# Kernel tuning notes

Measured on AMD Instinct MI355X. Metric: run time of the kernel, lower is better.

Reference implementation:

```python
import jax, jax.numpy as jnp
import numpy as np

NEG_SLOPE = 0.2
EPS = 1e-16


def setup_inputs() -> dict:
    key = jax.random.key(0)
    k1, k2, k3, k4, k5 = jax.random.split(key, 5)
    N, E, F_IN, H, C = 100000, 1600000, 128, 4, 32
    x = jax.random.normal(k1, (N, F_IN), dtype=jnp.float32)
    edge_index = jax.random.randint(k2, (2, E), 0, N, dtype=jnp.int64)
    W = jax.random.normal(k3, (F_IN, H * C), dtype=jnp.float32) * (1.0 / np.sqrt(F_IN))
    att_src = jax.random.normal(k4, (H, C), dtype=jnp.float32) * 0.1
    att_dst = jax.random.normal(k5, (H, C), dtype=jnp.float32) * 0.1
    bias = jnp.zeros((H * C,), dtype=jnp.float32)
    return {"x": x, "edge_index": edge_index, "W": W, "att_src": att_src,
            "att_dst": att_dst, "bias": bias}


def reference(x, edge_index, W, att_src, att_dst, bias):
    N = x.shape[0]
    H, C = att_src.shape
    # PyG GATConv default: add self-loops
    loops = jnp.arange(N, dtype=edge_index.dtype)
    src = jnp.concatenate([edge_index[0], loops])  # [E+N]
    dst = jnp.concatenate([edge_index[1], loops])  # [E+N]

    h = (x @ W).reshape(N, H, C)                  # [N,H,C]
    a_src = jnp.einsum('nhc,hc->nh', h, att_src)  # [N,H]
    a_dst = jnp.einsum('nhc,hc->nh', h, att_dst)  # [N,H]

    e = a_src[src] + a_dst[dst]                   # [E',H]
    e = jax.nn.leaky_relu(e, NEG_SLOPE)

    # segment softmax over destination nodes (numerically stable)
    m = jax.ops.segment_max(e, dst, num_segments=N)      # [N,H]
    p = jnp.exp(e - m[dst])                               # [E',H]
    s = jax.ops.segment_sum(p, dst, num_segments=N)       # [N,H]
    alpha = p / (s[dst] + EPS)                             # [E',H]

    msg = h[src] * alpha[:, :, None]                       # [E',H,C]
    out = jax.ops.segment_sum(msg, dst, num_segments=N)   # [N,H,C]
    return out.reshape(N, H * C) + bias
```

## Files before the change

kernel.cpp:

```cpp
#include <hip/hip_runtime.h>
#include <stdint.h>


#define SLOT 64
#define CNTS 16

typedef __attribute__((ext_vector_type(8))) _Float16 h8;
typedef __attribute__((ext_vector_type(4))) float    f4x;

__device__ __forceinline__ float b2f(unsigned short u) {
    union { unsigned int i; float f; } v; v.i = ((unsigned int)u) << 16; return v.f;
}
__device__ __forceinline__ unsigned short f2b(float f) {
    union { float f; unsigned int i; } v; v.f = f;
    unsigned int i = v.i;
    unsigned int r = (i + 0x7FFFu + ((i >> 16) & 1u)) >> 16;
    return (unsigned short)r;
}
__device__ __forceinline__ unsigned short f2h(float f) {
    union { _Float16 h; unsigned short u; } v; v.h = (_Float16)f; return v.u;
}
__device__ __forceinline__ float h2f(unsigned short u) {
    union { _Float16 h; unsigned short u; } v; v.u = u; return (float)v.h;
}

__global__ void k_detect(const int* __restrict__ eidx, const unsigned int* __restrict__ xw,
                         int* flags) {
    __shared__ int nz, bf;
    if (threadIdx.x == 0) { nz = 0; bf = 0; }
    __syncthreads();
    int bad = 0;
    for (int i = threadIdx.x; i < 1024; i += 256)
        if (eidx[2 * i + 1] != 0) bad = 1;
    if (bad) atomicOr(&nz, 1);
    int hits = 0;
    for (int i = threadIdx.x; i < 4096; i += 256) {
        unsigned int e = (xw[i] >> 7) & 0xFFu;
        if (e >= 0x60u && e < 0xA0u) ++hits;
    }
    atomicAdd(&bf, hits);
    __syncthreads();
    if (threadIdx.x == 0) {
        flags[0] = (nz == 0) ? 1 : 0;
        flags[1] = (bf > 3072) ? 1 : 0;
    }
}

__device__ __forceinline__ int edge_at(const int* idx32, const long long* idx64,
                                       int is64, long long pos) {
    return is64 ? (int)idx64[pos] : idx32[pos];
}

__global__ void k_prep(const void* __restrict__ Wv, const void* __restrict__ asv,
                       const void* __restrict__ adv, const void* __restrict__ bv,
                       const int* __restrict__ flags,
                       _Float16* __restrict__ Wth, _Float16* __restrict__ Wtl,
                       float* __restrict__ attf , float* __restrict__ biasf ) {
    int isbf = flags[1];
    int tid = blockIdx.x * 256 + threadIdx.x;
    for (int i = tid; i < 16384; i += gridDim.x * 256) {
        int col = i >> 7, k = i & 127;
        float w = isbf ? b2f(((const unsigned short*)Wv)[k * 128 + col])
                       : ((const float*)Wv)[k * 128 + col];
        unsigned short hi = f2h(w);
        unsigned short lo = f2h(w - h2f(hi));
        ((unsigned short*)Wth)[i] = hi;
        ((unsigned short*)Wtl)[i] = lo;
    }
    if (blockIdx.x == 0) {
        for (int i = threadIdx.x; i < 128; i += 256) {
            attf[i]       = isbf ? b2f(((const unsigned short*)asv)[i]) : ((const float*)asv)[i];
            attf[128 + i] = isbf ? b2f(((const unsigned short*)adv)[i]) : ((const float*)adv)[i];
            biasf[i]      = isbf ? b2f(((const unsigned short*)bv)[i]) : ((const float*)bv)[i];
        }
    }
}

__global__ __launch_bounds__(256) void k_gemm_scatter(
    const void* __restrict__ xv,
    const _Float16* __restrict__ Wth, const _Float16* __restrict__ Wtl,
    const float* __restrict__ attf, const int* __restrict__ flags,
    unsigned short* __restrict__ hbf, float* __restrict__ asf,
    float* __restrict__ adf, int N,
    const int* __restrict__ idx32, const long long* __restrict__ idx64,
    int* __restrict__ cnt, int* __restrict__ esrc, int E, int Gg, int Gs) {
    __shared__ unsigned short xsh[64 * 128];
    __shared__ unsigned short xsl[64 * 128];
    int role = blockIdx.x & 1, rb = blockIdx.x >> 1;
    int tid = threadIdx.x;

    if (role == 1) {
        if (rb >= Gs) return;
        int is64 = flags[0];
        int base = (rb * 256 + tid) * 4;
        if (base + 3 < E) {
            int s0, s1, s2, s3, d0, d1, d2, d3;
            if (is64) {
                s0 = (int)idx64[base];     s1 = (int)idx64[base + 1];
                s2 = (int)idx64[base + 2]; s3 = (int)idx64[base + 3];
                d0 = (int)idx64[(long long)E + base];     d1 = (int)idx64[(long long)E + base + 1];
                d2 = (int)idx64[(long long)E + base + 2]; d3 = (int)idx64[(long long)E + base + 3];
            } else if ((E & 3) == 0) {
                int4 sv = *(const int4*)(idx32 + base);
                int4 dv = *(const int4*)(idx32 + E + base);
                s0 = sv.x; s1 = sv.y; s2 = sv.z; s3 = sv.w;
                d0 = dv.x; d1 = dv.y; d2 = dv.z; d3 = dv.w;
            } else {
                s0 = idx32[base];     s1 = idx32[base + 1];
                s2 = idx32[base + 2]; s3 = idx32[base + 3];
                d0 = idx32[E + base];     d1 = idx32[E + base + 1];
                d2 = idx32[E + base + 2]; d3 = idx32[E + base + 3];
            }
            int p0 = atomicAdd(&cnt[(size_t)d0 * CNTS], 1);
            int p1 = atomicAdd(&cnt[(size_t)d1 * CNTS], 1);
            int p2 = atomicAdd(&cnt[(size_t)d2 * CNTS], 1);
            int p3 = atomicAdd(&cnt[(size_t)d3 * CNTS], 1);
            if (p0 < SLOT) esrc[(size_t)d0 * SLOT + p0] = s0;
            if (p1 < SLOT) esrc[(size_t)d1 * SLOT + p1] = s1;
            if (p2 < SLOT) esrc[(size_t)d2 * SLOT + p2] = s2;
            if (p3 < SLOT) esrc[(size_t)d3 * SLOT + p3] = s3;
        } else {
            for (int e = base; e < E; ++e) {
                int s = edge_at(idx32, idx64, is64, e);
                int d = edge_at(idx32, idx64, is64, (long long)E + e);
                int p = atomicAdd(&cnt[(size_t)d * CNTS], 1);
                if (p < SLOT) esrc[(size_t)d * SLOT + p] = s;
            }
        }
        return;
    }

    if (rb >= Gg) return;
    int r0 = rb * 64;
    int isbf = flags[1];
    int w = tid >> 6;
    int lane = tid & 63;
    int li = lane & 15;
    int g  = lane >> 4;
    int c0 = w * 32;

    h8 Bh[2][4], Bl[2][4];
#pragma unroll
    for (int t = 0; t < 2; ++t)
#pragma unroll
        for (int s = 0; s < 4; ++s) {
            size_t o = (size_t)(c0 + 16 * t + li) * 128 + 32 * s + 8 * g;
            Bh[t][s] = *(const h8*)(Wth + o);
            Bl[t][s] = *(const h8*)(Wtl + o);
        }

#pragma unroll
    for (int it = 0; it < 4; ++it) {
        int idx = it * 2048 + tid * 8;
        int r = idx >> 7, k = idx & 127;
        int gr = r0 + r; if (gr >= N) gr = N - 1;
        float v[8];
        if (isbf) {
            uint4 raw = *(const uint4*)((const unsigned short*)xv + (size_t)gr * 128 + k);
            v[0] = b2f((unsigned short)(raw.x & 0xFFFFu)); v[1] = b2f((unsigned short)(raw.x >> 16));
            v[2] = b2f((unsigned short)(raw.y & 0xFFFFu)); v[3] = b2f((unsigned short)(raw.y >> 16));
            v[4] = b2f((unsigned short)(raw.z & 0xFFFFu)); v[5] = b2f((unsigned short)(raw.z >> 16));
            v[6] = b2f((unsigned short)(raw.w & 0xFFFFu)); v[7] = b2f((unsigned short)(raw.w >> 16));
        } else {
            const float* xf = (const float*)xv;
            float4 a = *(const float4*)(xf + (size_t)gr * 128 + k);
            float4 b = *(const float4*)(xf + (size_t)gr * 128 + k + 4);
            v[0] = a.x; v[1] = a.y; v[2] = a.z; v[3] = a.w;
            v[4] = b.x; v[5] = b.y; v[6] = b.z; v[7] = b.w;
        }
        uint4 PH, PL;
        unsigned int ph[4], pl[4];
#pragma unroll
        for (int jj = 0; jj < 4; ++jj) {
            unsigned short h0 = f2h(v[2 * jj]), h1 = f2h(v[2 * jj + 1]);
            unsigned short l0 = f2h(v[2 * jj] - h2f(h0));
            unsigned short l1 = f2h(v[2 * jj + 1] - h2f(h1));
            ph[jj] = (unsigned int)h0 | ((unsigned int)h1 << 16);
            pl[jj] = (unsigned int)l0 | ((unsigned int)l1 << 16);
        }
        PH.x = ph[0]; PH.y = ph[1]; PH.z = ph[2]; PH.w = ph[3];
        PL.x = pl[0]; PL.y = pl[1]; PL.z = pl[2]; PL.w = pl[3];
        int off = r * 256 + ((2 * k) ^ ((r & 7) << 4));
        *(uint4*)((char*)xsh + off) = PH;
        *(uint4*)((char*)xsl + off) = PL;
    }
    __syncthreads();

    f4x acc[4][2];
#pragma unroll
    for (int m = 0; m < 4; ++m)
#pragma unroll
        for (int t = 0; t < 2; ++t) acc[m][t] = (f4x){0.f, 0.f, 0.f, 0.f};

#pragma unroll
    for (int s = 0; s < 4; ++s) {
#pragma unroll
        for (int m = 0; m < 4; ++m) {
            int row = 16 * m + li;
            int kb = (32 * s + 8 * g) * 2;
            int off = row * 256 + (kb ^ ((row & 7) << 4));
            h8 ah = *(const h8*)((const char*)xsh + off);
            h8 al = *(const h8*)((const char*)xsl + off);
#pragma unroll
            for (int t = 0; t < 2; ++t) {
                acc[m][t] = __builtin_amdgcn_mfma_f32_16x16x32_f16(ah, Bh[t][s], acc[m][t], 0, 0, 0);
                acc[m][t] = __builtin_amdgcn_mfma_f32_16x16x32_f16(al, Bh[t][s], acc[m][t], 0, 0, 0);
                acc[m][t] = __builtin_amdgcn_mfma_f32_16x16x32_f16(ah, Bl[t][s], acc[m][t], 0, 0, 0);
            }
        }
    }

    float at_s0 = attf[c0 + li],       at_s1 = attf[c0 + 16 + li];
    float at_d0 = attf[128 + c0 + li], at_d1 = attf[128 + c0 + 16 + li];
#pragma unroll
    for (int m = 0; m < 4; ++m) {
        float s1v[4], s2v[4];
#pragma unroll
        for (int j = 0; j < 4; ++j) {
            s1v[j] = acc[m][0][j] * at_s0 + acc[m][1][j] * at_s1;
            s2v[j] = acc[m][0][j] * at_d0 + acc[m][1][j] * at_d1;
        }
#pragma unroll
        for (int j = 0; j < 4; ++j) {
#pragma unroll
            for (int msk = 1; msk < 16; msk <<= 1) {
                s1v[j] += __shfl_xor(s1v[j], msk);
                s2v[j] += __shfl_xor(s2v[j], msk);
            }
        }
        if (li == 0) {
#pragma unroll
            for (int j = 0; j < 4; ++j) {
                int gr = r0 + 16 * m + 4 * g + j;
                if (gr < N) {
                    asf[(size_t)gr * 4 + w] = s1v[j];
                    adf[(size_t)gr * 4 + w] = s2v[j];
                }
            }
        }
    }

    __syncthreads();
#pragma unroll
    for (int m = 0; m < 4; ++m)
#pragma unroll
        for (int t = 0; t < 2; ++t)
#pragma unroll
            for (int j = 0; j < 4; ++j)
                xsh[(16 * m + 4 * g + j) * 128 + c0 + 16 * t + li] = f2b(acc[m][t][j]);
    __syncthreads();
#pragma unroll
    for (int it = 0; it < 4; ++it) {
        int u = it * 2048 + tid * 8;
        int r = u >> 7, k = u & 127;
        int gr = r0 + r;
        if (gr < N)
            *(uint4*)(hbf + (size_t)gr * 128 + k) = *(const uint4*)(xsh + u);
    }
}

__global__ __launch_bounds__(256) void k_aggregate(
    const unsigned short* __restrict__ hbf,
    const float* __restrict__ asf, const float* __restrict__ adf,
    const int* __restrict__ cnt, const int* __restrict__ esrc,
    const int* __restrict__ idx32, const long long* __restrict__ idx64,
    const float* __restrict__ biasf, const int* __restrict__ flags,
    void* __restrict__ outv, int N, int E) {
    __shared__ float p_sh_all[4][SLOT * 4];
    __shared__ int   s_sh_all[4][SLOT];
    int wid = threadIdx.x >> 6;
    int lane = threadIdx.x & 63;
    int n = blockIdx.x * 4 + wid;
    if (n >= N) n = N - 1;
    float* p_sh = p_sh_all[wid];
    int*   s_sh = s_sh_all[wid];
    int head = lane >> 4;

    int deg = cnt[(size_t)n * CNTS];
    float4 adv = *(const float4*)(adf + (size_t)n * 4);
    bool fb = (deg > SLOT - 1);

    float p0 = 0.f, p1 = 0.f, p2 = 0.f, p3 = 0.f;
    if (!fb && lane <= deg) {
        int s = (lane == 0) ? n : esrc[(size_t)n * SLOT + lane - 1];
        float4 av = *(const float4*)(asf + (size_t)s * 4);
        float e0 = av.x + adv.x; e0 = fmaxf(e0, 0.2f * e0); p0 = __expf(e0);
        float e1 = av.y + adv.y; e1 = fmaxf(e1, 0.2f * e1); p1 = __expf(e1);
        float e2 = av.z + adv.z; e2 = fmaxf(e2, 0.2f * e2); p2 = __expf(e2);
        float e3 = av.w + adv.w; e3 = fmaxf(e3, 0.2f * e3); p3 = __expf(e3);
        s_sh[lane] = s;
        p_sh[lane * 4 + 0] = p0; p_sh[lane * 4 + 1] = p1;
        p_sh[lane * 4 + 2] = p2; p_sh[lane * 4 + 3] = p3;
    }
    __syncthreads();

    float b0 = biasf[2 * lane], b1 = biasf[2 * lane + 1];
    float a0 = 0.f, a1 = 0.f, invh;

    if (!fb) {
        float ps0 = p0, ps1 = p1, ps2 = p2, ps3 = p3;
#pragma unroll
        for (int m = 1; m < 64; m <<= 1) {
            ps0 += __shfl_xor(ps0, m);
            ps1 += __shfl_xor(ps1, m);
            ps2 += __shfl_xor(ps2, m);
            ps3 += __shfl_xor(ps3, m);
        }
        float den = head == 0 ? ps0 : head == 1 ? ps1 : head == 2 ? ps2 : ps3;
        invh = 1.0f / (den + 1e-16f);

        int tot = deg + 1;
        int i = 0;
        for (; i + 3 < tot; i += 4) {
            int s0 = s_sh[i], s1 = s_sh[i + 1], s2 = s_sh[i + 2], s3 = s_sh[i + 3];
            float q0 = p_sh[i * 4 + head],       q1 = p_sh[(i + 1) * 4 + head];
            float q2 = p_sh[(i + 2) * 4 + head], q3 = p_sh[(i + 3) * 4 + head];
            unsigned int v0 = *(const unsigned int*)(hbf + (size_t)s0 * 128 + 2 * lane);
            unsigned int v1 = *(const unsigned int*)(hbf + (size_t)s1 * 128 + 2 * lane);
            unsigned int v2 = *(const unsigned int*)(hbf + (size_t)s2 * 128 + 2 * lane);
            unsigned int v3 = *(const unsigned int*)(hbf + (size_t)s3 * 128 + 2 * lane);
            a0 += q0 * b2f((unsigned short)v0) + q1 * b2f((unsigned short)v1)
                + q2 * b2f((unsigned short)v2) + q3 * b2f((unsigned short)v3);
            a1 += q0 * b2f((unsigned short)(v0 >> 16)) + q1 * b2f((unsigned short)(v1 >> 16))
                + q2 * b2f((unsigned short)(v2 >> 16)) + q3 * b2f((unsigned short)(v3 >> 16));
        }
        for (; i < tot; ++i) {
            int s0 = s_sh[i];
            float q0 = p_sh[i * 4 + head];
            unsigned int v0 = *(const unsigned int*)(hbf + (size_t)s0 * 128 + 2 * lane);
            a0 += q0 * b2f((unsigned short)v0);
            a1 += q0 * b2f((unsigned short)(v0 >> 16));
        }
    } else {
        int is64 = flags[0];
        float adh = head == 0 ? adv.x : head == 1 ? adv.y : head == 2 ? adv.z : adv.w;
        float den = 0.f;
        {
            float ev = asf[(size_t)n * 4 + head] + adh; ev = fmaxf(ev, 0.2f * ev);
            float p = __expf(ev);
            unsigned int v = *(const unsigned int*)(hbf + (size_t)n * 128 + 2 * lane);
            den += p;
            a0 += p * b2f((unsigned short)v);
            a1 += p * b2f((unsigned short)(v >> 16));
        }
        for (int e = 0; e < E; ++e) {
            int d = edge_at(idx32, idx64, is64, (long long)E + e);
            if (d == n) {
                int s = edge_at(idx32, idx64, is64, e);
                float ev = asf[(size_t)s * 4 + head] + adh; ev = fmaxf(ev, 0.2f * ev);
                float p = __expf(ev);
                unsigned int v = *(const unsigned int*)(hbf + (size_t)s * 128 + 2 * lane);
                den += p;
                a0 += p * b2f((unsigned short)v);
                a1 += p * b2f((unsigned short)(v >> 16));
            }
        }
        invh = 1.0f / (den + 1e-16f);
    }

    a0 = a0 * invh + b0;
    a1 = a1 * invh + b1;
    if (flags[1]) {
        unsigned int pk = (unsigned int)f2b(a0) | ((unsigned int)f2b(a1) << 16);
        ((unsigned int*)outv)[(size_t)n * 64 + lane] = pk;
    } else {
        float2 f2; f2.x = a0; f2.y = a1;
        *(float2*)((float*)outv + (size_t)n * 128 + 2 * lane) = f2;
    }
}

extern "C" void kernel_launch(void* const* d_in, const int* in_sizes, int n_in,
                              void* d_out, int out_size, void* d_ws, size_t ws_size,
                              hipStream_t stream) {
    const void*      xv    = d_in[0];
    const int*       idx32 = (const int*)d_in[1];
    const long long* idx64 = (const long long*)d_in[1];

    int N = in_sizes[0] / 128;
    int E = in_sizes[1] / 2;

    char* ws = (char*)d_ws;
    size_t o = 0;
    auto alloc = [&](size_t bytes) {
        size_t r = o; o += (bytes + 255) & ~(size_t)255; return r;
    };
    unsigned short* hbf = (unsigned short*)(ws + alloc((size_t)N * 128 * 2));
    _Float16* Wth = (_Float16*)(ws + alloc(16384 * 2));
    _Float16* Wtl = (_Float16*)(ws + alloc(16384 * 2));
    float* attf  = (float*)(ws + alloc(256 * 4));
    float* biasf = (float*)(ws + alloc(128 * 4));
    float* asf   = (float*)(ws + alloc((size_t)N * 4 * 4));
    float* adf   = (float*)(ws + alloc((size_t)N * 4 * 4));
    int* cnt     = (int*)(ws + alloc((size_t)N * CNTS * 4));
    int* flags   = (int*)(ws + alloc(256));
    int* esrc    = (int*)(ws + alloc((size_t)N * SLOT * 4));

    int Gg = (N + 63) / 64;
    int Gs = (E / 4 + 255) / 256;
    int G2 = (Gg > Gs ? Gg : Gs);

    k_detect<<<1, 256, 0, stream>>>(idx32, (const unsigned int*)xv, flags);
    k_prep<<<16, 256, 0, stream>>>(d_in[2], d_in[3], d_in[4], d_in[5], flags, Wth, Wtl, attf, biasf);
    hipMemsetAsync(cnt, 0, (size_t)N * CNTS * 4, stream);
    k_gemm_scatter<<<2 * G2, 256, 0, stream>>>(xv, Wth, Wtl, attf, flags, hbf, asf, adf, N,
                                               idx32, idx64, cnt, esrc, E, Gg, Gs);
    k_aggregate<<<(N + 3) / 4, 256, 0, stream>>>(hbf, asf, adf, cnt, esrc, idx32, idx64,
                                                 biasf, flags, d_out, N, E);
}
```

Before: 281.3 us.

## Partition edge scatter by destination range across 8 blocks per edge chunk

The edge-bucketing role of the fused GEMM/scatter kernel now gives each edge chunk to 8 blocks. Each block owns one eighth of the destination node range and only does atomics and esrc writes for destinations in its range. This keeps each block's scattered atomic and store traffic in a smaller address window, which should improve cache/L2 locality and reduce contention. In exchange, the destination indices are read 8 times over, adding extra global reads and branch divergence.

```diff
diff --git a/kernel.cpp b/kernel.cpp
--- a/kernel.cpp
+++ b/kernel.cpp
@@ -83,53 +83,71 @@
     unsigned short* __restrict__ hbf, float* __restrict__ asf,
     float* __restrict__ adf, int N,
     const int* __restrict__ idx32, const long long* __restrict__ idx64,
-    int* __restrict__ cnt, int* __restrict__ esrc, int E, int Gg, int Gs) {
+    int* __restrict__ cnt, int* __restrict__ esrc, int E, int Gg, int CH) {
     __shared__ unsigned short xsh[64 * 128];
     __shared__ unsigned short xsl[64 * 128];
-    int role = blockIdx.x & 1, rb = blockIdx.x >> 1;
+    int cell = blockIdx.x >> 4;
+    int slot = blockIdx.x & 15;
     int tid = threadIdx.x;
 
-    if (role == 1) {
-        if (rb >= Gs) return;
+    if (slot < 8) {
+        int gpart = slot;
+        long long e0 = (long long)cell * CH;
+        if (e0 >= E) return;
+        long long e1 = e0 + CH; if (e1 > E) e1 = E;
         int is64 = flags[0];
-        int base = (rb * 256 + tid) * 4;
-        if (base + 3 < E) {
-            int s0, s1, s2, s3, d0, d1, d2, d3;
-            if (is64) {
-                s0 = (int)idx64[base];     s1 = (int)idx64[base + 1];
-                s2 = (int)idx64[base + 2]; s3 = (int)idx64[base + 3];
-                d0 = (int)idx64[(long long)E + base];     d1 = (int)idx64[(long long)E + base + 1];
-                d2 = (int)idx64[(long long)E + base + 2]; d3 = (int)idx64[(long long)E + base + 3];
-            } else if ((E & 3) == 0) {
-                int4 sv = *(const int4*)(idx32 + base);
-                int4 dv = *(const int4*)(idx32 + E + base);
-                s0 = sv.x; s1 = sv.y; s2 = sv.z; s3 = sv.w;
-                d0 = dv.x; d1 = dv.y; d2 = dv.z; d3 = dv.w;
+        int NS = (N + 7) >> 3;
+        unsigned lo = (unsigned)(gpart * NS);
+        bool al = ((E & 3) == 0) && !is64;
+
+        for (long long base = e0 + tid * 4; base < e1; base += 1024) {
+            if (base + 3 < e1) {
+                int d0, d1, d2, d3;
+                if (is64) {
+                    d0 = (int)idx64[E + base];     d1 = (int)idx64[E + base + 1];
+                    d2 = (int)idx64[E + base + 2]; d3 = (int)idx64[E + base + 3];
+                } else if (al) {
+                    int4 dv = *(const int4*)(idx32 + E + base);
+                    d0 = dv.x; d1 = dv.y; d2 = dv.z; d3 = dv.w;
+                } else {
+                    d0 = idx32[E + base];     d1 = idx32[E + base + 1];
+                    d2 = idx32[E + base + 2]; d3 = idx32[E + base + 3];
+                }
+                if ((unsigned)(d0 - lo) < (unsigned)NS) {
+                    int s0 = is64 ? (int)idx64[base] : idx32[base];
+                    int p0 = atomicAdd(&cnt[(size_t)d0 * CNTS], 1);
+                    if (p0 < SLOT) esrc[(size_t)d0 * SLOT + p0] = s0;
+                }
+                if ((unsigned)(d1 - lo) < (unsigned)NS) {
+                    int s1 = is64 ? (int)idx64[base + 1] : idx32[base + 1];
+                    int p1 = atomicAdd(&cnt[(size_t)d1 * CNTS], 1);
+                    if (p1 < SLOT) esrc[(size_t)d1 * SLOT + p1] = s1;
+                }
+                if ((unsigned)(d2 - lo) < (unsigned)NS) {
+                    int s2 = is64 ? (int)idx64[base + 2] : idx32[base + 2];
+                    int p2 = atomicAdd(&cnt[(size_t)d2 * CNTS], 1);
+                    if (p2 < SLOT) esrc[(size_t)d2 * SLOT + p2] = s2;
+                }
+                if ((unsigned)(d3 - lo) < (unsigned)NS) {
+                    int s3 = is64 ? (int)idx64[base + 3] : idx32[base + 3];
+                    int p3 = atomicAdd(&cnt[(size_t)d3 * CNTS], 1);
+                    if (p3 < SLOT) esrc[(size_t)d3 * SLOT + p3] = s3;
+                }
             } else {
-                s0 = idx32[base];     s1 = idx32[base + 1];
-                s2 = idx32[base + 2]; s3 = idx32[base + 3];
-                d0 = idx32[E + base];     d1 = idx32[E + base + 1];
-                d2 = idx32[E + base + 2]; d3 = idx32[E + base + 3];
+                for (long long e = base; e < e1; ++e) {
+                    int d = edge_at(idx32, idx64, is64, (long long)E + e);
+                    if ((unsigned)(d - lo) < (unsigned)NS) {
+                        int s = edge_at(idx32, idx64, is64, e);
+                        int p = atomicAdd(&cnt[(size_t)d * CNTS], 1);
+                        if (p < SLOT) esrc[(size_t)d * SLOT + p] = s;
+                    }
+                }
             }
-            int p0 = atomicAdd(&cnt[(size_t)d0 * CNTS], 1);
-            int p1 = atomicAdd(&cnt[(size_t)d1 * CNTS], 1);
-            int p2 = atomicAdd(&cnt[(size_t)d2 * CNTS], 1);
-            int p3 = atomicAdd(&cnt[(size_t)d3 * CNTS], 1);
-            if (p0 < SLOT) esrc[(size_t)d0 * SLOT + p0] = s0;
-            if (p1 < SLOT) esrc[(size_t)d1 * SLOT + p1] = s1;
-            if (p2 < SLOT) esrc[(size_t)d2 * SLOT + p2] = s2;
-            if (p3 < SLOT) esrc[(size_t)d3 * SLOT + p3] = s3;
-        } else {
-            for (int e = base; e < E; ++e) {
-                int s = edge_at(idx32, idx64, is64, e);
-                int d = edge_at(idx32, idx64, is64, (long long)E + e);
-                int p = atomicAdd(&cnt[(size_t)d * CNTS], 1);
-                if (p < SLOT) esrc[(size_t)d * SLOT + p] = s;
-            }
         }
         return;
     }
 
+    int rb = cell * 8 + (slot - 8);
     if (rb >= Gg) return;
     int r0 = rb * 64;
     int isbf = flags[1];
@@ -396,14 +414,17 @@
     int* esrc    = (int*)(ws + alloc((size_t)N * SLOT * 4));
 
     int Gg = (N + 63) / 64;
-    int Gs = (E / 4 + 255) / 256;
-    int G2 = (Gg > Gs ? Gg : Gs);
+    int cells = (Gg + 7) / 8;
+    long long ch = ((long long)E + cells - 1) / cells;
+    int CH = (int)((ch + 1023) & ~1023LL);
+    if (CH < 1024) CH = 1024;
+    int NB = 16 * cells;
 
     k_detect<<<1, 256, 0, stream>>>(idx32, (const unsigned int*)xv, flags);
     k_prep<<<16, 256, 0, stream>>>(d_in[2], d_in[3], d_in[4], d_in[5], flags, Wth, Wtl, attf, biasf);
     hipMemsetAsync(cnt, 0, (size_t)N * CNTS * 4, stream);
-    k_gemm_scatter<<<2 * G2, 256, 0, stream>>>(xv, Wth, Wtl, attf, flags, hbf, asf, adf, N,
-                                               idx32, idx64, cnt, esrc, E, Gg, Gs);
+    k_gemm_scatter<<<NB, 256, 0, stream>>>(xv, Wth, Wtl, attf, flags, hbf, asf, adf, N,
+                                           idx32, idx64, cnt, esrc, E, Gg, CH);
     k_aggregate<<<(N + 3) / 4, 256, 0, stream>>>(hbf, asf, adf, cnt, esrc, idx32, idx64,
                                                  biasf, flags, d_out, N, E);
 }
```

After: 306.1 us. 8.8% more time.

## Replace per-edge global atomics with two-pass bucketed edge scatter and demux

Applied to the files above, without the earlier changes.

Edge bucketing switches from one global atomic per edge on per-node counters to a two-level scheme. Each block builds a shared-memory histogram over 64-node buckets, reserves ranges with one global atomic per bucket, and writes packed (src, local dst) entries. A new demux kernel then sorts each bucket into per-node slots in shared memory and writes esrc/cnt with coalesced stores. This cuts global atomic contention and scattered writes, at the cost of an extra kernel launch and an extra pass over the edges. Src indices are packed into 26 bits, and a bucket that overflows its fixed capacity is flagged to the aggregate kernel as overflow.

```diff
diff --git a/kernel.cpp b/kernel.cpp
--- a/kernel.cpp
+++ b/kernel.cpp
@@ -4,6 +4,9 @@
 
 #define SLOT 64
 #define CNTS 16
+#define BCAP 1536
+#define MAXB 2048
+#define KCH  16384
 
 typedef __attribute__((ext_vector_type(8))) _Float16 h8;
 typedef __attribute__((ext_vector_type(4))) float    f4x;
@@ -83,46 +86,51 @@
     unsigned short* __restrict__ hbf, float* __restrict__ asf,
     float* __restrict__ adf, int N,
     const int* __restrict__ idx32, const long long* __restrict__ idx64,
-    int* __restrict__ cnt, int* __restrict__ esrc, int E, int Gg, int Gs) {
+    int* __restrict__ bcnt, unsigned* __restrict__ bdat,
+    int* __restrict__ cnt, int* __restrict__ esrc,
+    int E, int Gg, int SB) {
     __shared__ unsigned short xsh[64 * 128];
     __shared__ unsigned short xsl[64 * 128];
-    int role = blockIdx.x & 1, rb = blockIdx.x >> 1;
     int tid = threadIdx.x;
-
-    if (role == 1) {
-        if (rb >= Gs) return;
+    int bid = blockIdx.x;
+
+    if (bid < SB) {
         int is64 = flags[0];
-        int base = (rb * 256 + tid) * 4;
-        if (base + 3 < E) {
-            int s0, s1, s2, s3, d0, d1, d2, d3;
-            if (is64) {
-                s0 = (int)idx64[base];     s1 = (int)idx64[base + 1];
-                s2 = (int)idx64[base + 2]; s3 = (int)idx64[base + 3];
-                d0 = (int)idx64[(long long)E + base];     d1 = (int)idx64[(long long)E + base + 1];
-                d2 = (int)idx64[(long long)E + base + 2]; d3 = (int)idx64[(long long)E + base + 3];
-            } else if ((E & 3) == 0) {
-                int4 sv = *(const int4*)(idx32 + base);
-                int4 dv = *(const int4*)(idx32 + E + base);
-                s0 = sv.x; s1 = sv.y; s2 = sv.z; s3 = sv.w;
-                d0 = dv.x; d1 = dv.y; d2 = dv.z; d3 = dv.w;
-            } else {
-                s0 = idx32[base];     s1 = idx32[base + 1];
-                s2 = idx32[base + 2]; s3 = idx32[base + 3];
-                d0 = idx32[E + base];     d1 = idx32[E + base + 1];
-                d2 = idx32[E + base + 2]; d3 = idx32[E + base + 3];
-            }
-            int p0 = atomicAdd(&cnt[(size_t)d0 * CNTS], 1);
-            int p1 = atomicAdd(&cnt[(size_t)d1 * CNTS], 1);
-            int p2 = atomicAdd(&cnt[(size_t)d2 * CNTS], 1);
-            int p3 = atomicAdd(&cnt[(size_t)d3 * CNTS], 1);
-            if (p0 < SLOT) esrc[(size_t)d0 * SLOT + p0] = s0;
-            if (p1 < SLOT) esrc[(size_t)d1 * SLOT + p1] = s1;
-            if (p2 < SLOT) esrc[(size_t)d2 * SLOT + p2] = s2;
-            if (p3 < SLOT) esrc[(size_t)d3 * SLOT + p3] = s3;
+        int NBK = (N + 63) >> 6;
+        long long e0 = (long long)bid * KCH;
+        long long e1 = e0 + KCH; if (e1 > E) e1 = E;
+        if (e0 >= E) return;
+
+        if (NBK <= MAXB) {
+            int* hist = (int*)xsh;
+            for (int i = tid; i < NBK; i += 256) hist[i] = 0;
+            __syncthreads();
+            for (long long e = e0 + tid; e < e1; e += 256) {
+                int d = is64 ? (int)idx64[(long long)E + e] : idx32[E + e];
+                atomicAdd(&hist[d >> 6], 1);
+            }
+            __syncthreads();
+            for (int b = tid; b < NBK; b += 256) {
+                int c = hist[b];
+                hist[b] = (c > 0) ? atomicAdd(&bcnt[b], c) : 0;
+            }
+            __syncthreads();
+            for (long long e = e0 + tid; e < e1; e += 256) {
+                int d, s;
+                if (is64) {
+                    d = (int)idx64[(long long)E + e]; s = (int)idx64[e];
+                } else {
+                    d = idx32[E + e]; s = idx32[e];
+                }
+                int b = d >> 6;
+                int p = atomicAdd(&hist[b], 1);
+                if (p < BCAP)
+                    bdat[(size_t)b * BCAP + p] = (unsigned)s | ((unsigned)(d & 63) << 26);
+            }
         } else {
-            for (int e = base; e < E; ++e) {
+            for (long long e = e0 + tid; e < e1; e += 256) {
+                int d = edge_at(idx32, idx64, is64, (long long)E + e);
                 int s = edge_at(idx32, idx64, is64, e);
-                int d = edge_at(idx32, idx64, is64, (long long)E + e);
                 int p = atomicAdd(&cnt[(size_t)d * CNTS], 1);
                 if (p < SLOT) esrc[(size_t)d * SLOT + p] = s;
             }
@@ -130,6 +138,7 @@
         return;
     }
 
+    int rb = bid - SB;
     if (rb >= Gg) return;
     int r0 = rb * 64;
     int isbf = flags[1];
@@ -259,6 +268,37 @@
     }
 }
 
+__global__ __launch_bounds__(256) void k_demux(
+    const unsigned* __restrict__ bdat, const int* __restrict__ bcnt,
+    int* __restrict__ cnt, int* __restrict__ esrc, int N) {
+    __shared__ int lcnt[64];
+    __shared__ int lslot[64][64];
+    int b = blockIdx.x;
+    int tid = threadIdx.x;
+    if (tid < 64) lcnt[tid] = 0;
+    __syncthreads();
+    int m = bcnt[b];
+    int ovf = (m > BCAP);
+    if (m > BCAP) m = BCAP;
+    for (int i = tid; i < m; i += 256) {
+        unsigned e = bdat[(size_t)b * BCAP + i];
+        int dl = (int)(e >> 26);
+        int s  = (int)(e & 0x03FFFFFFu);
+        int p = atomicAdd(&lcnt[dl], 1);
+        if (p < SLOT) lslot[dl][p] = s;
+    }
+    __syncthreads();
+    int n0 = b << 6;
+    for (int i = tid; i < 1024; i += 256) {
+        int row = i >> 4;
+        if (n0 + row < N)
+            *(int4*)(esrc + (size_t)(n0 + row) * SLOT + (i & 15) * 4) =
+                ((const int4*)lslot)[i];
+    }
+    if (tid < 64 && n0 + tid < N)
+        cnt[(size_t)(n0 + tid) * CNTS] = ovf ? (SLOT + 1) : lcnt[tid];
+}
+
 __global__ __launch_bounds__(256) void k_aggregate(
     const unsigned short* __restrict__ hbf,
     const float* __restrict__ asf, const float* __restrict__ adf,
@@ -394,16 +434,26 @@
     int* cnt     = (int*)(ws + alloc((size_t)N * CNTS * 4));
     int* flags   = (int*)(ws + alloc(256));
     int* esrc    = (int*)(ws + alloc((size_t)N * SLOT * 4));
+    int NBK = (N + 63) >> 6;
+    int* bcnt      = (int*)(ws + alloc((size_t)NBK * 4));
+    unsigned* bdat = (unsigned*)(ws + alloc((size_t)NBK * BCAP * 4));
 
     int Gg = (N + 63) / 64;
-    int Gs = (E / 4 + 255) / 256;
-    int G2 = (Gg > Gs ? Gg : Gs);
+    int SB = (E + KCH - 1) / KCH;
+    int NB = SB + Gg;
 
     k_detect<<<1, 256, 0, stream>>>(idx32, (const unsigned int*)xv, flags);
     k_prep<<<16, 256, 0, stream>>>(d_in[2], d_in[3], d_in[4], d_in[5], flags, Wth, Wtl, attf, biasf);
-    hipMemsetAsync(cnt, 0, (size_t)N * CNTS * 4, stream);
-    k_gemm_scatter<<<2 * G2, 256, 0, stream>>>(xv, Wth, Wtl, attf, flags, hbf, asf, adf, N,
-                                               idx32, idx64, cnt, esrc, E, Gg, Gs);
+    if (NBK <= MAXB) {
+        hipMemsetAsync(bcnt, 0, (size_t)NBK * 4, stream);
+        k_gemm_scatter<<<NB, 256, 0, stream>>>(xv, Wth, Wtl, attf, flags, hbf, asf, adf, N,
+                                               idx32, idx64, bcnt, bdat, cnt, esrc, E, Gg, SB);
+        k_demux<<<NBK, 256, 0, stream>>>(bdat, bcnt, cnt, esrc, N);
+    } else {
+        hipMemsetAsync(cnt, 0, (size_t)N * CNTS * 4, stream);
+        k_gemm_scatter<<<NB, 256, 0, stream>>>(xv, Wth, Wtl, attf, flags, hbf, asf, adf, N,
+                                               idx32, idx64, bcnt, bdat, cnt, esrc, E, Gg, SB);
+    }
     k_aggregate<<<(N + 3) / 4, 256, 0, stream>>>(hbf, asf, adf, cnt, esrc, idx32, idx64,
                                                  biasf, flags, d_out, N, E);
 }
```

New measurement: 271.7 us. 3.4% less time.
